# Kernel optimization log

Measured on AMD Instinct MI355X. Metric: run time of the kernel, lower is better.

Reference implementation:

```python
import jax, jax.numpy as jnp
import numpy as np
import math

SIGMA = 0.6  # bandwidths=[0.6]; torch code returns inside the loop so only the first sigma is used
GAMMA = math.gamma((SIGMA + 1.0) / 2.0) / (math.gamma(SIGMA / 2.0) * SIGMA ** 0.5)


def setup_inputs() -> dict:
    key = jax.random.key(0)
    k1, k2 = jax.random.split(key)
    X1 = jax.random.normal(k1, (4096, 128), dtype=jnp.float32)
    X2 = jax.random.normal(k2, (4096, 128), dtype=jnp.float32)
    return {"X1": X1, "X2": X2}


def _student_kernel(G, a_sq, b_sq):
    # G: [a,b] inner products; a_sq/b_sq: squared norms
    d2 = -2.0 * G + a_sq[:, None] + b_sq[None, :]
    return GAMMA * jnp.power(1.0 + d2 / 2.0, -(SIGMA + 1.0) / 2.0)


def _double_center(K):
    # CM @ K @ CM^T  ==  K - rowmean - colmean + totalmean (exact)
    cm = K.mean(axis=0, keepdims=True)  # mean over rows -> subtracted per column
    rm = K.mean(axis=1, keepdims=True)  # mean over cols -> subtracted per row
    tm = K.mean()
    return K - cm - rm + tm


def reference(X1, X2):
    m = X1.shape[0]
    n = X2.shape[0]
    XX = X1 @ X1.T
    XY = X1 @ X2.T
    YY = X2 @ X2.T
    x_sq = jnp.diagonal(XX)
    y_sq = jnp.diagonal(YY)
    K_XX = _student_kernel(XX, x_sq, x_sq)
    K_XY = _student_kernel(XY, x_sq, y_sq)
    K_YY = _student_kernel(YY, y_sq, y_sq)
    C_XX2 = jnp.square(_double_center(K_XX))
    C_XY2 = jnp.square(_double_center(K_XY))
    C_YY2 = jnp.square(_double_center(K_YY))
    # unbiased branch with const_diagonal = sum(wts) = 1 -> trace_X = m, trace_Y = n
    mf = jnp.float32(m)
    nf = jnp.float32(n)
    vdr2 = (jnp.sum(C_XX2) - mf) / ((mf - 1.0) * mf) \
         + (jnp.sum(C_YY2) - nf) / ((nf - 1.0) * nf) \
         - 2.0 * jnp.sum(C_XY2) / (mf * nf)
    return vdr2
```

## Files before the change

### kernel.cpp

```cpp
#include <hip/hip_runtime.h>


typedef __attribute__((ext_vector_type(8))) _Float16 f16x8;
typedef __attribute__((ext_vector_type(2))) _Float16 f16x2;
typedef __attribute__((ext_vector_type(4))) float f32x4;

#define GAMMA_F 0.50241665f
#define NTILES 8256
#define NWAVES 2048
#define SLAB (64 * 4096)

#define OFF_SQ1   0
#define OFF_SQ2   16384
#define OFF_H1    32768
#define OFF_H2    1081344
#define OFF_SLABS 2129920
#define OFF_BPART (2129920 + 4194304)
#define OFF_PARTA (OFF_BPART + 24576)

__global__ __launch_bounds__(256) void vdr_prep(const float* __restrict__ X1,
                                                const float* __restrict__ X2,
                                                _Float16* __restrict__ H1,
                                                _Float16* __restrict__ H2,
                                                float* __restrict__ sq1,
                                                float* __restrict__ sq2) {
  const int gw = (blockIdx.x * 256 + threadIdx.x) >> 6;
  const int lane = threadIdx.x & 63;
  const float* X; _Float16* H; float* SQ; int row;
  if (gw < 4096) { X = X1; H = H1; SQ = sq1; row = gw; }
  else           { X = X2; H = H2; SQ = sq2; row = gw - 4096; }
  const float2 v = reinterpret_cast<const float2*>(X + (size_t)row * 128)[lane];
  f16x2 h; h.x = (_Float16)v.x; h.y = (_Float16)v.y;
  reinterpret_cast<f16x2*>(H + (size_t)row * 128)[lane] = h;
  float s = v.x * v.x + v.y * v.y;
  #pragma unroll
  for (int o = 32; o; o >>= 1) s += __shfl_xor(s, o);
  if (lane == 0) SQ[row] = s;
}

__device__ __forceinline__ void tri_decode(int u, int& bi, int& bj) {
  int b = (int)(64.5f - sqrtf(4160.25f - 2.0f * (float)u));
  if (b < 0) b = 0; if (b > 63) b = 63;
  while (b > 0 && (b * (129 - b)) / 2 > u) --b;
  while (b < 63 && ((b + 1) * (128 - b)) / 2 <= u) ++b;
  bi = b;
  bj = b + (u - (b * (129 - b)) / 2);
}

__global__ __launch_bounds__(256) void vdr_main(const _Float16* __restrict__ H1,
                                                const _Float16* __restrict__ H2,
                                                const float* __restrict__ sq1,
                                                const float* __restrict__ sq2,
                                                float* __restrict__ slabs,
                                                float* __restrict__ bpart) {
  const int w = threadIdx.x >> 6, lane = threadIdx.x & 63;
  const int lr = lane & 15, lg = lane >> 4;
  const int gw = blockIdx.x * 4 + w;

  __shared__ float rs_area_s[4][16][65];
  __shared__ float colbuf_s[4][64];
  float (*rs_area)[65] = rs_area_s[w];
  float* colbuf = colbuf_s[w];

  float kxx = 0.f, kxy = 0.f, kyy = 0.f;

  int z, bi, bj; const _Float16 *A, *B; const float *as, *bs;
  auto decode = [&](int T, int& z_, int& bi_, int& bj_, const _Float16*& A_,
                    const _Float16*& B_, const float*& as_, const float*& bs_) {
    if (T < 2080)      { z_ = 0; tri_decode(T, bi_, bj_);          A_ = H1; B_ = H1; as_ = sq1; bs_ = sq1; }
    else if (T < 6176) { z_ = 1; int v = T - 2080; bi_ = v >> 6; bj_ = v & 63;
                                                                   A_ = H1; B_ = H2; as_ = sq1; bs_ = sq2; }
    else               { z_ = 2; tri_decode(T - 6176, bi_, bj_);   A_ = H2; B_ = H2; as_ = sq2; bs_ = sq2; }
  };

  int t = gw;
  decode(t, z, bi, bj, A, B, as, bs);

  f16x8 pa[4], pb[4];
  {
    const int ko = lg * 8;
    #pragma unroll
    for (int mi = 0; mi < 4; ++mi)
      pa[mi] = *reinterpret_cast<const f16x8*>(A + (size_t)(bi * 64 + mi * 16 + lr) * 128 + ko);
    #pragma unroll
    for (int ni = 0; ni < 4; ++ni)
      pb[ni] = *reinterpret_cast<const f16x8*>(B + (size_t)(bj * 64 + ni * 16 + lr) * 128 + ko);
  }

  while (t < NTILES) {
    f32x4 acc[4][4];
    #pragma unroll
    for (int mi = 0; mi < 4; ++mi)
      #pragma unroll
      for (int ni = 0; ni < 4; ++ni)
        acc[mi][ni] = (f32x4){0.f, 0.f, 0.f, 0.f};

    #pragma unroll
    for (int mi = 0; mi < 4; ++mi)
      #pragma unroll
      for (int ni = 0; ni < 4; ++ni)
        acc[mi][ni] = __builtin_amdgcn_mfma_f32_16x16x32_f16(pa[mi], pb[ni], acc[mi][ni], 0, 0, 0);

    #pragma unroll
    for (int ks = 1; ks < 4; ++ks) {
      const int ko = ks * 32 + lg * 8;
      f16x8 a[4], b[4];
      #pragma unroll
      for (int mi = 0; mi < 4; ++mi)
        a[mi] = *reinterpret_cast<const f16x8*>(A + (size_t)(bi * 64 + mi * 16 + lr) * 128 + ko);
      #pragma unroll
      for (int ni = 0; ni < 4; ++ni)
        b[ni] = *reinterpret_cast<const f16x8*>(B + (size_t)(bj * 64 + ni * 16 + lr) * 128 + ko);
      #pragma unroll
      for (int mi = 0; mi < 4; ++mi)
        #pragma unroll
        for (int ni = 0; ni < 4; ++ni)
          acc[mi][ni] = __builtin_amdgcn_mfma_f32_16x16x32_f16(a[mi], b[ni], acc[mi][ni], 0, 0, 0);
    }

    const int tn = t + NWAVES;
    const bool more = tn < NTILES;
    int zn, bin, bjn; const _Float16 *An = A, *Bn = B; const float *asn = as, *bsn = bs;
    if (more) {
      decode(tn, zn, bin, bjn, An, Bn, asn, bsn);
      const int ko = lg * 8;
      #pragma unroll
      for (int mi = 0; mi < 4; ++mi)
        pa[mi] = *reinterpret_cast<const f16x8*>(An + (size_t)(bin * 64 + mi * 16 + lr) * 128 + ko);
      #pragma unroll
      for (int ni = 0; ni < 4; ++ni)
        pb[ni] = *reinterpret_cast<const f16x8*>(Bn + (size_t)(bjn * 64 + ni * 16 + lr) * 128 + ko);
    }
    __builtin_amdgcn_sched_barrier(0);

    float cb[4];
    #pragma unroll
    for (int ni = 0; ni < 4; ++ni) cb[ni] = 0.5f * bs[bj * 64 + ni * 16 + lr];
    const bool dg = (z != 1) && (bi == bj);
    float tk = 0.f;
    float cpart[4] = {0.f, 0.f, 0.f, 0.f};

    #pragma unroll
    for (int mi = 0; mi < 4; ++mi) {
      const float4 aq = *reinterpret_cast<const float4*>(as + bi * 64 + mi * 16 + lg * 4);
      const float aqv[4] = {aq.x, aq.y, aq.z, aq.w};
      #pragma unroll
      for (int rg = 0; rg < 4; ++rg) {
        const float pre = __builtin_fmaf(0.5f, aqv[rg], 1.0f);
        float rp = 0.f;
        #pragma unroll
        for (int ni = 0; ni < 4; ++ni) {
          const float G = acc[mi][ni][rg];
          const float base = (pre + cb[ni]) - G;
          float Kv = GAMMA_F * __builtin_amdgcn_exp2f(-0.8f * __builtin_amdgcn_logf(base));
          if (dg) { if ((mi * 16 + lg * 4 + rg) == (ni * 16 + lr)) Kv = GAMMA_F; }
          rp += Kv;
          cpart[ni] += Kv;
          tk = __builtin_fmaf(Kv, Kv, tk);
        }
        rs_area[lr][mi * 16 + lg * 4 + rg] = rp;
      }
    }
    const float wt = (z != 1 && bi != bj) ? 2.f : 1.f;
    if (z == 0) kxx = __builtin_fmaf(wt, tk, kxx);
    else if (z == 1) kxy += tk;
    else kyy = __builtin_fmaf(wt, tk, kyy);

    float rsum = 0.f;
    #pragma unroll
    for (int j = 0; j < 16; ++j) rsum += rs_area[j][lane];

    #pragma unroll
    for (int ni = 0; ni < 4; ++ni) {
      float cp = cpart[ni];
      cp += __shfl_xor(cp, 16);
      cp += __shfl_xor(cp, 32);
      if (lg == 0) colbuf[ni * 16 + lr] = cp;
    }
    const float cval = colbuf[lane];

    float* rowslab = slabs + (size_t)((z == 0) ? 0 : (z == 1) ? 1 : 3) * SLAB;
    rowslab[(size_t)bj * 4096 + bi * 64 + lane] = rsum;
    if (z == 1)
      slabs[(size_t)2 * SLAB + (size_t)bi * 4096 + bj * 64 + lane] = cval;
    else if (bi != bj)
      rowslab[(size_t)bi * 4096 + bj * 64 + lane] = cval;

    if (more) { z = zn; bi = bin; bj = bjn; A = An; B = Bn; as = asn; bs = bsn; }
    t = tn;
  }

  #pragma unroll
  for (int o = 32; o; o >>= 1) {
    kxx += __shfl_xor(kxx, o);
    kxy += __shfl_xor(kxy, o);
    kyy += __shfl_xor(kyy, o);
  }
  if (lane == 0) {
    bpart[gw] = kxx;
    bpart[2048 + gw] = kxy;
    bpart[4096 + gw] = kyy;
  }
}

__global__ __launch_bounds__(256) void vdr_reduceA(const float* __restrict__ slabs,
                                                   double* __restrict__ partA) {
  const int j = blockIdx.y, tid = threadIdx.x;
  const int e = blockIdx.x * 256 + tid;
  const float* base = slabs + (size_t)j * SLAB + e;
  double s = 0.0;
  #pragma unroll
  for (int k = 0; k < 64; ++k) s += (double)base[(size_t)k * 4096];
  double sq = s * s, sm = s;
  #pragma unroll
  for (int o = 32; o; o >>= 1) { sq += __shfl_down(sq, o); sm += __shfl_down(sm, o); }
  __shared__ double sh[4][2];
  const int lane = tid & 63, wid = tid >> 6;
  if (lane == 0) { sh[wid][0] = sq; sh[wid][1] = sm; }
  __syncthreads();
  if (tid == 0) {
    partA[(size_t)(j * 16 + blockIdx.x) * 2 + 0] = sh[0][0] + sh[1][0] + sh[2][0] + sh[3][0];
    partA[(size_t)(j * 16 + blockIdx.x) * 2 + 1] = sh[0][1] + sh[1][1] + sh[2][1] + sh[3][1];
  }
}

__global__ __launch_bounds__(256) void vdr_reduceB(const double* __restrict__ partA,
                                                   const float* __restrict__ bpart,
                                                   float* __restrict__ out) {
  const int tid = threadIdx.x;
  __shared__ double ssq[4], ssum[4], s2sh[4][3];
  double s2[3] = {0.0, 0.0, 0.0};
  for (int i = tid; i < 2048; i += 256) {
    s2[0] += (double)bpart[i];
    s2[1] += (double)bpart[2048 + i];
    s2[2] += (double)bpart[4096 + i];
  }
  #pragma unroll
  for (int o = 32; o; o >>= 1) {
    s2[0] += __shfl_down(s2[0], o);
    s2[1] += __shfl_down(s2[1], o);
    s2[2] += __shfl_down(s2[2], o);
  }
  const int lane = tid & 63, wid = tid >> 6;
  if (lane == 0) { s2sh[wid][0] = s2[0]; s2sh[wid][1] = s2[1]; s2sh[wid][2] = s2[2]; }
  if (tid < 64) {
    const int j = tid >> 4, c = tid & 15;
    double sq = partA[(size_t)(j * 16 + c) * 2 + 0];
    double sm = partA[(size_t)(j * 16 + c) * 2 + 1];
    #pragma unroll
    for (int o = 8; o; o >>= 1) { sq += __shfl_down(sq, o, 16); sm += __shfl_down(sm, o, 16); }
    if (c == 0) { ssq[j] = sq; ssum[j] = sm; }
  }
  __syncthreads();
  if (tid == 0) {
    const double S2XX = s2sh[0][0] + s2sh[1][0] + s2sh[2][0] + s2sh[3][0];
    const double S2XY = s2sh[0][1] + s2sh[1][1] + s2sh[2][1] + s2sh[3][1];
    const double S2YY = s2sh[0][2] + s2sh[1][2] + s2sh[2][2] + s2sh[3][2];
    const double inv = 1.0 / 4096.0;
    const double r0 = S2XX - 2.0 * ssq[0] * inv + ssum[0] * ssum[0] * inv * inv;
    const double r1 = S2XY - ssq[1] * inv - ssq[2] * inv + ssum[1] * ssum[1] * inv * inv;
    const double r2 = S2YY - 2.0 * ssq[3] * inv + ssum[3] * ssum[3] * inv * inv;
    const double mf = 4096.0;
    out[0] = (float)((r0 - mf) / ((mf - 1.0) * mf)
                   + (r2 - mf) / ((mf - 1.0) * mf)
                   - 2.0 * r1 / (mf * mf));
  }
}

extern "C" void kernel_launch(void* const* d_in, const int* in_sizes, int n_in,
                              void* d_out, int out_size, void* d_ws, size_t ws_size,
                              hipStream_t stream) {
  const float* X1 = (const float*)d_in[0];
  const float* X2 = (const float*)d_in[1];
  char* ws = (char*)d_ws;
  float* sq1      = (float*)(ws + OFF_SQ1);
  float* sq2      = (float*)(ws + OFF_SQ2);
  _Float16* H1    = (_Float16*)(ws + OFF_H1);
  _Float16* H2    = (_Float16*)(ws + OFF_H2);
  float* slabs    = (float*)(ws + OFF_SLABS);
  float* bpart    = (float*)(ws + OFF_BPART);
  double* partA   = (double*)(ws + OFF_PARTA);

  vdr_prep<<<2048, 256, 0, stream>>>(X1, X2, H1, H2, sq1, sq2);
  vdr_main<<<512, 256, 0, stream>>>(H1, H2, sq1, sq2, slabs, bpart);
  dim3 ga(16, 4);
  vdr_reduceA<<<ga, 256, 0, stream>>>(slabs, partA);
  vdr_reduceB<<<1, 256, 0, stream>>>(partA, bpart, (float*)d_out);
}
```

Baseline: 57.70 us.

## Replace persistent tile loop with one wave per tile and per-tile partials

The persistent-wave kernel, which looped over tiles with a software-prefetched first K-slice, becomes a kernel that launches one wave per 64x64 tile (2064 blocks), with launch_bounds asking for more resident blocks. Each wave writes its own weighted sum of squares to bpart, and the final reduction classifies the entries by tile index. The GAMMA multiply is folded into the exponent as a log2 offset inside an fma. This trades the cross-tile load/compute overlap for more waves in flight and simpler code, at the cost of more block launches and a larger partial buffer.

```diff
diff --git a/kernel.cpp b/kernel.cpp
--- a/kernel.cpp
+++ b/kernel.cpp
@@ -5,9 +5,9 @@
 typedef __attribute__((ext_vector_type(2))) _Float16 f16x2;
 typedef __attribute__((ext_vector_type(4))) float f32x4;
 
+#define LOG2G (-0.99304426f)
 #define GAMMA_F 0.50241665f
 #define NTILES 8256
-#define NWAVES 2048
 #define SLAB (64 * 4096)
 
 #define OFF_SQ1   0
@@ -16,7 +16,7 @@
 #define OFF_H2    1081344
 #define OFF_SLABS 2129920
 #define OFF_BPART (2129920 + 4194304)
-#define OFF_PARTA (OFF_BPART + 24576)
+#define OFF_PARTA (OFF_BPART + 33024)
 
 __global__ __launch_bounds__(256) void vdr_prep(const float* __restrict__ X1,
                                                 const float* __restrict__ X2,
@@ -47,159 +47,107 @@
   bj = b + (u - (b * (129 - b)) / 2);
 }
 
-__global__ __launch_bounds__(256) void vdr_main(const _Float16* __restrict__ H1,
-                                                const _Float16* __restrict__ H2,
-                                                const float* __restrict__ sq1,
-                                                const float* __restrict__ sq2,
-                                                float* __restrict__ slabs,
-                                                float* __restrict__ bpart) {
+__global__ __launch_bounds__(256, 4) void vdr_main(const _Float16* __restrict__ H1,
+                                                   const _Float16* __restrict__ H2,
+                                                   const float* __restrict__ sq1,
+                                                   const float* __restrict__ sq2,
+                                                   float* __restrict__ slabs,
+                                                   float* __restrict__ bpart) {
   const int w = threadIdx.x >> 6, lane = threadIdx.x & 63;
   const int lr = lane & 15, lg = lane >> 4;
-  const int gw = blockIdx.x * 4 + w;
+  const int t = blockIdx.x * 4 + w;
 
   __shared__ float rs_area_s[4][16][65];
   __shared__ float colbuf_s[4][64];
   float (*rs_area)[65] = rs_area_s[w];
   float* colbuf = colbuf_s[w];
 
-  float kxx = 0.f, kxy = 0.f, kyy = 0.f;
-
   int z, bi, bj; const _Float16 *A, *B; const float *as, *bs;
-  auto decode = [&](int T, int& z_, int& bi_, int& bj_, const _Float16*& A_,
-                    const _Float16*& B_, const float*& as_, const float*& bs_) {
-    if (T < 2080)      { z_ = 0; tri_decode(T, bi_, bj_);          A_ = H1; B_ = H1; as_ = sq1; bs_ = sq1; }
-    else if (T < 6176) { z_ = 1; int v = T - 2080; bi_ = v >> 6; bj_ = v & 63;
-                                                                   A_ = H1; B_ = H2; as_ = sq1; bs_ = sq2; }
-    else               { z_ = 2; tri_decode(T - 6176, bi_, bj_);   A_ = H2; B_ = H2; as_ = sq2; bs_ = sq2; }
-  };
-
-  int t = gw;
-  decode(t, z, bi, bj, A, B, as, bs);
-
-  f16x8 pa[4], pb[4];
-  {
-    const int ko = lg * 8;
+  if (t < 2080)      { z = 0; tri_decode(t, bi, bj);        A = H1; B = H1; as = sq1; bs = sq1; }
+  else if (t < 6176) { z = 1; int v = t - 2080; bi = v >> 6; bj = v & 63;
+                                                            A = H1; B = H2; as = sq1; bs = sq2; }
+  else               { z = 2; tri_decode(t - 6176, bi, bj); A = H2; B = H2; as = sq2; bs = sq2; }
+
+  f32x4 acc[4][4];
+  #pragma unroll
+  for (int mi = 0; mi < 4; ++mi)
+    #pragma unroll
+    for (int ni = 0; ni < 4; ++ni)
+      acc[mi][ni] = (f32x4){0.f, 0.f, 0.f, 0.f};
+
+  #pragma unroll
+  for (int ks = 0; ks < 4; ++ks) {
+    const int ko = ks * 32 + lg * 8;
+    f16x8 a[4], b[4];
     #pragma unroll
     for (int mi = 0; mi < 4; ++mi)
-      pa[mi] = *reinterpret_cast<const f16x8*>(A + (size_t)(bi * 64 + mi * 16 + lr) * 128 + ko);
+      a[mi] = *reinterpret_cast<const f16x8*>(A + (size_t)(bi * 64 + mi * 16 + lr) * 128 + ko);
     #pragma unroll
     for (int ni = 0; ni < 4; ++ni)
-      pb[ni] = *reinterpret_cast<const f16x8*>(B + (size_t)(bj * 64 + ni * 16 + lr) * 128 + ko);
-  }
-
-  while (t < NTILES) {
-    f32x4 acc[4][4];
+      b[ni] = *reinterpret_cast<const f16x8*>(B + (size_t)(bj * 64 + ni * 16 + lr) * 128 + ko);
     #pragma unroll
     for (int mi = 0; mi < 4; ++mi)
       #pragma unroll
       for (int ni = 0; ni < 4; ++ni)
-        acc[mi][ni] = (f32x4){0.f, 0.f, 0.f, 0.f};
-
-    #pragma unroll
-    for (int mi = 0; mi < 4; ++mi)
+        acc[mi][ni] = __builtin_amdgcn_mfma_f32_16x16x32_f16(a[mi], b[ni], acc[mi][ni], 0, 0, 0);
+  }
+
+  float cb[4];
+  #pragma unroll
+  for (int ni = 0; ni < 4; ++ni) cb[ni] = 0.5f * bs[bj * 64 + ni * 16 + lr];
+  const bool dg = (z != 1) && (bi == bj);
+
+  float k2s = 0.f;
+  float cpart[4] = {0.f, 0.f, 0.f, 0.f};
+
+  #pragma unroll
+  for (int mi = 0; mi < 4; ++mi) {
+    const float4 aq = *reinterpret_cast<const float4*>(as + bi * 64 + mi * 16 + lg * 4);
+    const float aqv[4] = {aq.x, aq.y, aq.z, aq.w};
+    #pragma unroll
+    for (int rg = 0; rg < 4; ++rg) {
+      const float pre = __builtin_fmaf(0.5f, aqv[rg], 1.0f);
+      float rp = 0.f;
       #pragma unroll
-      for (int ni = 0; ni < 4; ++ni)
-        acc[mi][ni] = __builtin_amdgcn_mfma_f32_16x16x32_f16(pa[mi], pb[ni], acc[mi][ni], 0, 0, 0);
-
-    #pragma unroll
-    for (int ks = 1; ks < 4; ++ks) {
-      const int ko = ks * 32 + lg * 8;
-      f16x8 a[4], b[4];
-      #pragma unroll
-      for (int mi = 0; mi < 4; ++mi)
-        a[mi] = *reinterpret_cast<const f16x8*>(A + (size_t)(bi * 64 + mi * 16 + lr) * 128 + ko);
-      #pragma unroll
-      for (int ni = 0; ni < 4; ++ni)
-        b[ni] = *reinterpret_cast<const f16x8*>(B + (size_t)(bj * 64 + ni * 16 + lr) * 128 + ko);
-      #pragma unroll
-      for (int mi = 0; mi < 4; ++mi)
-        #pragma unroll
-        for (int ni = 0; ni < 4; ++ni)
-          acc[mi][ni] = __builtin_amdgcn_mfma_f32_16x16x32_f16(a[mi], b[ni], acc[mi][ni], 0, 0, 0);
+      for (int ni = 0; ni < 4; ++ni) {
+        const float G = acc[mi][ni][rg];
+        const float base = (pre + cb[ni]) - G;
+        float Kv = __builtin_amdgcn_exp2f(
+            __builtin_fmaf(-0.8f, __builtin_amdgcn_logf(base), LOG2G));
+        if (dg) { if ((mi * 16 + lg * 4 + rg) == (ni * 16 + lr)) Kv = GAMMA_F; }
+        rp += Kv;
+        cpart[ni] += Kv;
+        k2s = __builtin_fmaf(Kv, Kv, k2s);
+      }
+      rs_area[lr][mi * 16 + lg * 4 + rg] = rp;
     }
-
-    const int tn = t + NWAVES;
-    const bool more = tn < NTILES;
-    int zn, bin, bjn; const _Float16 *An = A, *Bn = B; const float *asn = as, *bsn = bs;
-    if (more) {
-      decode(tn, zn, bin, bjn, An, Bn, asn, bsn);
-      const int ko = lg * 8;
-      #pragma unroll
-      for (int mi = 0; mi < 4; ++mi)
-        pa[mi] = *reinterpret_cast<const f16x8*>(An + (size_t)(bin * 64 + mi * 16 + lr) * 128 + ko);
-      #pragma unroll
-      for (int ni = 0; ni < 4; ++ni)
-        pb[ni] = *reinterpret_cast<const f16x8*>(Bn + (size_t)(bjn * 64 + ni * 16 + lr) * 128 + ko);
-    }
-    __builtin_amdgcn_sched_barrier(0);
-
-    float cb[4];
-    #pragma unroll
-    for (int ni = 0; ni < 4; ++ni) cb[ni] = 0.5f * bs[bj * 64 + ni * 16 + lr];
-    const bool dg = (z != 1) && (bi == bj);
-    float tk = 0.f;
-    float cpart[4] = {0.f, 0.f, 0.f, 0.f};
-
-    #pragma unroll
-    for (int mi = 0; mi < 4; ++mi) {
-      const float4 aq = *reinterpret_cast<const float4*>(as + bi * 64 + mi * 16 + lg * 4);
-      const float aqv[4] = {aq.x, aq.y, aq.z, aq.w};
-      #pragma unroll
-      for (int rg = 0; rg < 4; ++rg) {
-        const float pre = __builtin_fmaf(0.5f, aqv[rg], 1.0f);
-        float rp = 0.f;
-        #pragma unroll
-        for (int ni = 0; ni < 4; ++ni) {
-          const float G = acc[mi][ni][rg];
-          const float base = (pre + cb[ni]) - G;
-          float Kv = GAMMA_F * __builtin_amdgcn_exp2f(-0.8f * __builtin_amdgcn_logf(base));
-          if (dg) { if ((mi * 16 + lg * 4 + rg) == (ni * 16 + lr)) Kv = GAMMA_F; }
-          rp += Kv;
-          cpart[ni] += Kv;
-          tk = __builtin_fmaf(Kv, Kv, tk);
-        }
-        rs_area[lr][mi * 16 + lg * 4 + rg] = rp;
-      }
-    }
+  }
+
+  float rsum = 0.f;
+  #pragma unroll
+  for (int j = 0; j < 16; ++j) rsum += rs_area[j][lane];
+
+  #pragma unroll
+  for (int ni = 0; ni < 4; ++ni) {
+    float cp = cpart[ni];
+    cp += __shfl_xor(cp, 16);
+    cp += __shfl_xor(cp, 32);
+    if (lg == 0) colbuf[ni * 16 + lr] = cp;
+  }
+  const float cval = colbuf[lane];
+
+  float* rowslab = slabs + (size_t)((z == 0) ? 0 : (z == 1) ? 1 : 3) * SLAB;
+  rowslab[(size_t)bj * 4096 + bi * 64 + lane] = rsum;
+  if (z == 1)
+    slabs[(size_t)2 * SLAB + (size_t)bi * 4096 + bj * 64 + lane] = cval;
+  else if (bi != bj)
+    rowslab[(size_t)bi * 4096 + bj * 64 + lane] = cval;
+
+  #pragma unroll
+  for (int o = 32; o; o >>= 1) k2s += __shfl_xor(k2s, o);
+  if (lane == 0) {
     const float wt = (z != 1 && bi != bj) ? 2.f : 1.f;
-    if (z == 0) kxx = __builtin_fmaf(wt, tk, kxx);
-    else if (z == 1) kxy += tk;
-    else kyy = __builtin_fmaf(wt, tk, kyy);
-
-    float rsum = 0.f;
-    #pragma unroll
-    for (int j = 0; j < 16; ++j) rsum += rs_area[j][lane];
-
-    #pragma unroll
-    for (int ni = 0; ni < 4; ++ni) {
-      float cp = cpart[ni];
-      cp += __shfl_xor(cp, 16);
-      cp += __shfl_xor(cp, 32);
-      if (lg == 0) colbuf[ni * 16 + lr] = cp;
-    }
-    const float cval = colbuf[lane];
-
-    float* rowslab = slabs + (size_t)((z == 0) ? 0 : (z == 1) ? 1 : 3) * SLAB;
-    rowslab[(size_t)bj * 4096 + bi * 64 + lane] = rsum;
-    if (z == 1)
-      slabs[(size_t)2 * SLAB + (size_t)bi * 4096 + bj * 64 + lane] = cval;
-    else if (bi != bj)
-      rowslab[(size_t)bi * 4096 + bj * 64 + lane] = cval;
-
-    if (more) { z = zn; bi = bin; bj = bjn; A = An; B = Bn; as = asn; bs = bsn; }
-    t = tn;
-  }
-
-  #pragma unroll
-  for (int o = 32; o; o >>= 1) {
-    kxx += __shfl_xor(kxx, o);
-    kxy += __shfl_xor(kxy, o);
-    kyy += __shfl_xor(kyy, o);
-  }
-  if (lane == 0) {
-    bpart[gw] = kxx;
-    bpart[2048 + gw] = kxy;
-    bpart[4096 + gw] = kyy;
+    bpart[t] = wt * k2s;
   }
 }
 
@@ -230,10 +178,9 @@
   const int tid = threadIdx.x;
   __shared__ double ssq[4], ssum[4], s2sh[4][3];
   double s2[3] = {0.0, 0.0, 0.0};
-  for (int i = tid; i < 2048; i += 256) {
-    s2[0] += (double)bpart[i];
-    s2[1] += (double)bpart[2048 + i];
-    s2[2] += (double)bpart[4096 + i];
+  for (int i = tid; i < NTILES; i += 256) {
+    const double v = (double)bpart[i];
+    if (i < 2080) s2[0] += v; else if (i < 6176) s2[1] += v; else s2[2] += v;
   }
   #pragma unroll
   for (int o = 32; o; o >>= 1) {
@@ -282,7 +229,7 @@
   double* partA   = (double*)(ws + OFF_PARTA);
 
   vdr_prep<<<2048, 256, 0, stream>>>(X1, X2, H1, H2, sq1, sq2);
-  vdr_main<<<512, 256, 0, stream>>>(H1, H2, sq1, sq2, slabs, bpart);
+  vdr_main<<<2064, 256, 0, stream>>>(H1, H2, sq1, sq2, slabs, bpart);
   dim3 ga(16, 4);
   vdr_reduceA<<<ga, 256, 0, stream>>>(slabs, partA);
   vdr_reduceB<<<1, 256, 0, stream>>>(partA, bpart, (float*)d_out);
```

After: 66.96 us. 1.16x slower.
